# Kernel optimization log

Hardware: AMD Instinct MI355X
Metric: run time of the kernel (lower is better)

Reference implementation:

```python
import jax, jax.numpy as jnp
import numpy as np

N = 8192
X_DIM = 256
Y_DIM = 256


def setup_inputs() -> dict:
    key = jax.random.key(0)
    kx, ky, kw = jax.random.split(key, 3)
    x_samples = jax.random.normal(kx, (N, X_DIM), dtype=jnp.float32)
    y_samples = jax.random.normal(ky, (N, Y_DIM), dtype=jnp.float32)
    # kaiming-uniform-ish init for the bilinear weight [x_dim, y_dim]
    bound = float(np.sqrt(6.0 / X_DIM))
    w = jax.random.uniform(kw, (X_DIM, Y_DIM), dtype=jnp.float32,
                           minval=-bound, maxval=bound)
    return {"x_samples": x_samples, "y_samples": y_samples, "w": w}


def reference(x_samples, y_samples, w):
    # Pairwise bilinear scores S[i, b] = x[i] @ W @ y[b]
    # (equivalent to the original's tiled einsum, without O(N^2*dim) tiles)
    n = y_samples.shape[0]
    xw = x_samples @ w                      # [N, y_dim]
    S = xw @ y_samples.T                    # [N, N], S[i, b]
    # T0[i] = S[i, i]; T1.logsumexp(dim=1)[b] = logsumexp_i S[i, b]
    t0_mean = jnp.mean(jnp.diagonal(S))
    lse_mean = jnp.mean(jax.nn.logsumexp(S, axis=0))
    lower_bound = t0_mean - (lse_mean - jnp.log(jnp.float32(n)))
    return lower_bound
```

## Files before the change

### kernel.cpp

```cpp
#include <hip/hip_runtime.h>

typedef __attribute__((ext_vector_type(8))) short bf16x8;
typedef __attribute__((ext_vector_type(4))) float f32x4;
typedef __attribute__((ext_vector_type(8))) int   i32x8;
typedef __attribute__((ext_vector_type(4))) int   i32x4;

union OpU { i32x8 v; i32x4 h[2]; };

__device__ __forceinline__ unsigned short f2bf(float f) {
    unsigned int u = __float_as_uint(f);
    u += 0x7fffu + ((u >> 16) & 1u);
    return (unsigned short)(u >> 16);
}

__global__ void cast_wy_kernel(const float* __restrict__ y, const float* __restrict__ w,
                               unsigned char* __restrict__ YQ, unsigned short* __restrict__ WT,
                               float* __restrict__ scal)
{
    int idx = blockIdx.x * 256 + threadIdx.x;
    const float4 yv = ((const float4*)y)[idx];
    int pk = __builtin_amdgcn_cvt_pk_fp8_f32(yv.x, yv.y, 0, 0);
    pk     = __builtin_amdgcn_cvt_pk_fp8_f32(yv.z, yv.w, pk, 1);
    ((int*)YQ)[idx] = pk;
    if (idx < 16384) {
        const float4 wv = ((const float4*)w)[idx];
        int k = idx >> 6;
        int n0 = (idx & 63) * 4;
        WT[(size_t)(n0 + 0) * 256 + k] = f2bf(wv.x);
        WT[(size_t)(n0 + 1) * 256 + k] = f2bf(wv.y);
        WT[(size_t)(n0 + 2) * 256 + k] = f2bf(wv.z);
        WT[(size_t)(n0 + 3) * 256 + k] = f2bf(wv.w);
    }
    if (idx == 0) {
        scal[0] = 0.f; scal[1] = 0.f;
        ((unsigned int*)scal)[2] = 0u;
    }
}

__global__ __launch_bounds__(256, 4)
void gemm0_kernel(const float* __restrict__ X, const unsigned short* __restrict__ WT,
                  unsigned char* __restrict__ XWQ)
{
    __shared__ __align__(16) unsigned short As[64 * 64];
    __shared__ __align__(16) unsigned short Bs[64 * 64];

    const int tid  = threadIdx.x;
    const int lane = tid & 63;
    const int w    = tid >> 6;
    const int wm   = w >> 1, wn = w & 1;
    const int frow = lane & 15, quad = lane >> 4;
    const int rowBase = blockIdx.y * 64;
    const int colBase = blockIdx.x * 64;

    int aOff[2][2], bOff[2][2];
#pragma unroll
    for (int mi = 0; mi < 2; ++mi)
#pragma unroll
        for (int kk = 0; kk < 2; ++kk) {
            int ka = kk * 4 + quad;
            int ra = wm * 32 + mi * 16 + frow;
            aOff[mi][kk] = ra * 64 + ((ka ^ (ra & 7)) << 3);
            int rb = wn * 32 + mi * 16 + frow;
            bOff[mi][kk] = rb * 64 + ((ka ^ (rb & 7)) << 3);
        }

    f32x4 acc[2][2];
#pragma unroll
    for (int i = 0; i < 2; ++i)
#pragma unroll
        for (int j = 0; j < 2; ++j)
            acc[i][j] = f32x4{0.f, 0.f, 0.f, 0.f};

#pragma unroll
    for (int kt = 0; kt < 4; ++kt) {
        const int k0 = kt * 64;
#pragma unroll
        for (int it = 0; it < 2; ++it) {
            int p  = it * 256 + tid;
            int r  = p >> 3;
            int s  = p & 7;
            int kc = s ^ (r & 7);
            const unsigned short* gb = WT + (size_t)(colBase + r) * 256 + k0 + (kc << 3);
            __builtin_amdgcn_global_load_lds(
                (const __attribute__((address_space(1))) void*)gb,
                (__attribute__((address_space(3))) void*)&Bs[p << 3], 16, 0, 0);
        }
#pragma unroll
        for (int it = 0; it < 4; ++it) {
            int fidx = it * 256 + tid;
            int r  = fidx >> 4;
            int c4 = fidx & 15;
            float4 v = *(const float4*)&X[(size_t)(rowBase + r) * 256 + k0 + c4 * 4];
            ushort4 u;
            u.x = f2bf(v.x); u.y = f2bf(v.y); u.z = f2bf(v.z); u.w = f2bf(v.w);
            int slot = (c4 >> 1) ^ (r & 7);
            *(ushort4*)&As[r * 64 + (slot << 3) + (c4 & 1) * 4] = u;
        }
        __syncthreads();
#pragma unroll
        for (int kk = 0; kk < 2; ++kk) {
            bf16x8 a[2], b[2];
#pragma unroll
            for (int mi = 0; mi < 2; ++mi) a[mi] = *(const bf16x8*)&As[aOff[mi][kk]];
#pragma unroll
            for (int ni = 0; ni < 2; ++ni) b[ni] = *(const bf16x8*)&Bs[bOff[ni][kk]];
#pragma unroll
            for (int mi = 0; mi < 2; ++mi)
#pragma unroll
                for (int ni = 0; ni < 2; ++ni)
                    acc[mi][ni] = __builtin_amdgcn_mfma_f32_16x16x32_bf16(
                        a[mi], b[ni], acc[mi][ni], 0, 0, 0);
        }
        __syncthreads();
    }

#pragma unroll
    for (int mi = 0; mi < 2; ++mi)
#pragma unroll
        for (int ni = 0; ni < 2; ++ni)
#pragma unroll
            for (int r2 = 0; r2 < 4; ++r2) {
                int row = rowBase + wm * 32 + mi * 16 + quad * 4 + r2;
                int col = colBase + wn * 32 + ni * 16 + frow;
                float v = acc[mi][ni][r2];
                int q = __builtin_amdgcn_cvt_pk_fp8_f32(v, v, 0, 0);
                XWQ[(size_t)row * 256 + col] = (unsigned char)(q & 0xff);
            }
}

__global__ __launch_bounds__(256, 3)
void gemm1_kernel(const unsigned char* __restrict__ A,
                  const unsigned char* __restrict__ B,
                  float* __restrict__ P, float* __restrict__ scal)
{
    __shared__ __align__(16) unsigned char As[128 * 128];
    __shared__ __align__(16) unsigned char Bs[128 * 128];
    __shared__ float lsebuf[256];

    const int tid  = threadIdx.x;
    const int lane = tid & 63;
    const int w    = tid >> 6;
    const int wm   = w >> 1, wn = w & 1;
    const int frow = lane & 15, quad = lane >> 4;
    const int rowBase = blockIdx.y * 128;
    const int colBase = blockIdx.x * 128;

    f32x4 acc[4][4];
#pragma unroll
    for (int i = 0; i < 4; ++i)
#pragma unroll
        for (int j = 0; j < 4; ++j)
            acc[i][j] = f32x4{0.f, 0.f, 0.f, 0.f};

#pragma unroll
    for (int kt = 0; kt < 2; ++kt) {
        const int k0 = kt * 128;
#pragma unroll
        for (int it = 0; it < 4; ++it) {
            int p  = it * 256 + tid;
            int r  = p >> 3;
            int s  = p & 7;
            int kc = s ^ (r & 7);
            const unsigned char* ga = A + (size_t)(rowBase + r) * 256 + k0 + (kc << 4);
            const unsigned char* gb = B + (size_t)(colBase + r) * 256 + k0 + (kc << 4);
            __builtin_amdgcn_global_load_lds(
                (const __attribute__((address_space(1))) void*)ga,
                (__attribute__((address_space(3))) void*)&As[p << 4], 16, 0, 0);
            __builtin_amdgcn_global_load_lds(
                (const __attribute__((address_space(1))) void*)gb,
                (__attribute__((address_space(3))) void*)&Bs[p << 4], 16, 0, 0);
        }
        __syncthreads();

        const int c0 = quad * 2;
        i32x8 a[4], b[4];
#pragma unroll
        for (int mi = 0; mi < 4; ++mi) {
            int ra = wm * 64 + mi * 16 + frow;
            OpU u;
            u.h[0] = *(const i32x4*)&As[ra * 128 + ((c0 ^ (ra & 7)) << 4)];
            u.h[1] = *(const i32x4*)&As[ra * 128 + (((c0 + 1) ^ (ra & 7)) << 4)];
            a[mi] = u.v;
        }
#pragma unroll
        for (int ni = 0; ni < 4; ++ni) {
            int rb = wn * 64 + ni * 16 + frow;
            OpU u;
            u.h[0] = *(const i32x4*)&Bs[rb * 128 + ((c0 ^ (rb & 7)) << 4)];
            u.h[1] = *(const i32x4*)&Bs[rb * 128 + (((c0 + 1) ^ (rb & 7)) << 4)];
            b[ni] = u.v;
        }
#pragma unroll
        for (int mi = 0; mi < 4; ++mi)
#pragma unroll
            for (int ni = 0; ni < 4; ++ni)
                acc[mi][ni] = __builtin_amdgcn_mfma_scale_f32_16x16x128_f8f6f4(
                    a[mi], b[ni], acc[mi][ni],
                    0, 0,
                    0, 0x7f7f7f7f,
                    0, 0x7f7f7f7f);
        __syncthreads();
    }

#pragma unroll
    for (int ni = 0; ni < 4; ++ni) {
        float m = -1e30f;
#pragma unroll
        for (int mi = 0; mi < 4; ++mi)
#pragma unroll
            for (int r2 = 0; r2 < 4; ++r2) m = fmaxf(m, acc[mi][ni][r2]);
        m = fmaxf(m, __shfl_xor(m, 16));
        m = fmaxf(m, __shfl_xor(m, 32));
        float ssum = 0.f;
#pragma unroll
        for (int mi = 0; mi < 4; ++mi)
#pragma unroll
            for (int r2 = 0; r2 < 4; ++r2) ssum += __expf(acc[mi][ni][r2] - m);
        ssum += __shfl_xor(ssum, 16);
        ssum += __shfl_xor(ssum, 32);
        if (quad == 0)
            lsebuf[wm * 128 + wn * 64 + ni * 16 + frow] = m + __logf(ssum);
    }
    if (blockIdx.x == blockIdx.y && wm == wn) {
        float v = 0.f;
#pragma unroll
        for (int mi = 0; mi < 4; ++mi)
#pragma unroll
            for (int r2 = 0; r2 < 4; ++r2)
                if (quad * 4 + r2 == frow) v += acc[mi][mi][r2];
#pragma unroll
        for (int o = 1; o < 64; o <<= 1) v += __shfl_xor(v, o);
        if (lane == 0) atomicAdd(&scal[0], v);
    }
    __syncthreads();
    if (tid < 128) {
        float a = lsebuf[tid], b = lsebuf[128 + tid];
        float mm = fmaxf(a, b);
        P[(size_t)blockIdx.y * 8192 + colBase + tid]
            = mm + __logf(__expf(a - mm) + __expf(b - mm));
    }
}

__global__ void combine_kernel(const float* __restrict__ P, float* __restrict__ scal,
                               float* __restrict__ out)
{
    __shared__ float red[256];
    const int tid = threadIdx.x;
    const int col = blockIdx.x * 256 + tid;
    float m = -1e30f, s = 0.f;
#pragma unroll 8
    for (int j = 0; j < 64; ++j) {
        float v = P[(size_t)j * 8192 + col];
        float nm = fmaxf(m, v);
        s = s * __expf(m - nm) + __expf(v - nm);
        m = nm;
    }
    red[tid] = m + logf(s);
    __syncthreads();
#pragma unroll
    for (int o = 128; o > 0; o >>= 1) {
        if (tid < o) red[tid] += red[tid + o];
        __syncthreads();
    }
    if (tid == 0) {
        atomicAdd(&scal[1], red[0]);
        __threadfence();
        unsigned int old = __hip_atomic_fetch_add((unsigned int*)&scal[2], 1u,
                                                  __ATOMIC_ACQ_REL, __HIP_MEMORY_SCOPE_AGENT);
        if (old == 31u) {
            float t0 = __hip_atomic_load(&scal[0], __ATOMIC_RELAXED, __HIP_MEMORY_SCOPE_AGENT);
            float ls = __hip_atomic_load(&scal[1], __ATOMIC_RELAXED, __HIP_MEMORY_SCOPE_AGENT);
            const float invN = 1.f / 8192.f;
            out[0] = t0 * invN - (ls * invN - logf(8192.f));
        }
    }
}

extern "C" void kernel_launch(void* const* d_in, const int* in_sizes, int n_in,
                              void* d_out, int out_size, void* d_ws, size_t ws_size,
                              hipStream_t stream)
{
    const float* x = (const float*)d_in[0];
    const float* y = (const float*)d_in[1];
    const float* w = (const float*)d_in[2];
    float* out = (float*)d_out;

    char* ws = (char*)d_ws;
    unsigned char*  YQ  = (unsigned char*)(ws);
    unsigned char*  XWQ = (unsigned char*)(ws + 0x200000);
    unsigned short* WT  = (unsigned short*)(ws + 0x400000);
    float*          P   = (float*)        (ws + 0x420000);
    float*          scal= (float*)        (ws + 0x620000);

    cast_wy_kernel<<<2048, 256, 0, stream>>>(y, w, YQ, WT, scal);
    gemm0_kernel<<<dim3(4, 128), 256, 0, stream>>>(x, WT, XWQ);
    gemm1_kernel<<<dim3(64, 64), 256, 0, stream>>>(XWQ, YQ, P, scal);
    combine_kernel<<<32, 256, 0, stream>>>(P, scal, out);
}
```

Before: 111.7 us.

## Fuse cast and combine kernels into the two GEMM kernels

```diff
diff --git a/kernel.cpp b/kernel.cpp
--- a/kernel.cpp
+++ b/kernel.cpp
@@ -13,33 +13,11 @@
     return (unsigned short)(u >> 16);
 }
 
-__global__ void cast_wy_kernel(const float* __restrict__ y, const float* __restrict__ w,
-                               unsigned char* __restrict__ YQ, unsigned short* __restrict__ WT,
-                               float* __restrict__ scal)
-{
-    int idx = blockIdx.x * 256 + threadIdx.x;
-    const float4 yv = ((const float4*)y)[idx];
-    int pk = __builtin_amdgcn_cvt_pk_fp8_f32(yv.x, yv.y, 0, 0);
-    pk     = __builtin_amdgcn_cvt_pk_fp8_f32(yv.z, yv.w, pk, 1);
-    ((int*)YQ)[idx] = pk;
-    if (idx < 16384) {
-        const float4 wv = ((const float4*)w)[idx];
-        int k = idx >> 6;
-        int n0 = (idx & 63) * 4;
-        WT[(size_t)(n0 + 0) * 256 + k] = f2bf(wv.x);
-        WT[(size_t)(n0 + 1) * 256 + k] = f2bf(wv.y);
-        WT[(size_t)(n0 + 2) * 256 + k] = f2bf(wv.z);
-        WT[(size_t)(n0 + 3) * 256 + k] = f2bf(wv.w);
-    }
-    if (idx == 0) {
-        scal[0] = 0.f; scal[1] = 0.f;
-        ((unsigned int*)scal)[2] = 0u;
-    }
-}
-
 __global__ __launch_bounds__(256, 4)
-void gemm0_kernel(const float* __restrict__ X, const unsigned short* __restrict__ WT,
-                  unsigned char* __restrict__ XWQ)
+void gemm0_kernel(const float* __restrict__ X, const float* __restrict__ W,
+                  const float* __restrict__ Y,
+                  unsigned char* __restrict__ XWQ, unsigned char* __restrict__ YQ,
+                  float* __restrict__ scal, unsigned int* __restrict__ tick)
 {
     __shared__ __align__(16) unsigned short As[64 * 64];
     __shared__ __align__(16) unsigned short Bs[64 * 64];
@@ -51,6 +29,21 @@
     const int frow = lane & 15, quad = lane >> 4;
     const int rowBase = blockIdx.y * 64;
     const int colBase = blockIdx.x * 64;
+    const int lb = blockIdx.y * 4 + blockIdx.x;
+
+    if (lb == 0 && tid == 0) {
+        scal[0] = 0.f; scal[1] = 0.f;
+        tick[0] = 0u;  tick[1] = 0u;
+    }
+
+#pragma unroll
+    for (int it = 0; it < 4; ++it) {
+        int idx = lb * 1024 + it * 256 + tid;
+        const float4 yv = ((const float4*)Y)[idx];
+        int pk = __builtin_amdgcn_cvt_pk_fp8_f32(yv.x, yv.y, 0, 0);
+        pk     = __builtin_amdgcn_cvt_pk_fp8_f32(yv.z, yv.w, pk, 1);
+        ((int*)YQ)[idx] = pk;
+    }
 
     int aOff[2][2], bOff[2][2];
 #pragma unroll
@@ -74,17 +67,6 @@
 #pragma unroll
     for (int kt = 0; kt < 4; ++kt) {
         const int k0 = kt * 64;
-#pragma unroll
-        for (int it = 0; it < 2; ++it) {
-            int p  = it * 256 + tid;
-            int r  = p >> 3;
-            int s  = p & 7;
-            int kc = s ^ (r & 7);
-            const unsigned short* gb = WT + (size_t)(colBase + r) * 256 + k0 + (kc << 3);
-            __builtin_amdgcn_global_load_lds(
-                (const __attribute__((address_space(1))) void*)gb,
-                (__attribute__((address_space(3))) void*)&Bs[p << 3], 16, 0, 0);
-        }
 #pragma unroll
         for (int it = 0; it < 4; ++it) {
             int fidx = it * 256 + tid;
@@ -96,6 +78,21 @@
             int slot = (c4 >> 1) ^ (r & 7);
             *(ushort4*)&As[r * 64 + (slot << 3) + (c4 & 1) * 4] = u;
         }
+#pragma unroll
+        for (int it = 0; it < 4; ++it) {
+            int fidx = it * 256 + tid;
+            int k  = fidx >> 4;
+            int c4 = fidx & 15;
+            float4 v = *(const float4*)&W[(size_t)(k0 + k) * 256 + colBase + c4 * 4];
+            int c = k >> 3;
+            int kl = k & 7;
+#pragma unroll
+            for (int j = 0; j < 4; ++j) {
+                int n = c4 * 4 + j;
+                float vj = (j == 0) ? v.x : (j == 1) ? v.y : (j == 2) ? v.z : v.w;
+                Bs[n * 64 + ((c ^ (n & 7)) << 3) + kl] = f2bf(vj);
+            }
+        }
         __syncthreads();
 #pragma unroll
         for (int kk = 0; kk < 2; ++kk) {
@@ -131,11 +128,13 @@
 __global__ __launch_bounds__(256, 3)
 void gemm1_kernel(const unsigned char* __restrict__ A,
                   const unsigned char* __restrict__ B,
-                  float* __restrict__ P, float* __restrict__ scal)
+                  float* __restrict__ P, float* __restrict__ scal,
+                  unsigned int* __restrict__ tick, float* __restrict__ out)
 {
     __shared__ __align__(16) unsigned char As[128 * 128];
     __shared__ __align__(16) unsigned char Bs[128 * 128];
     __shared__ float lsebuf[256];
+    __shared__ unsigned int tkS;
 
     const int tid  = threadIdx.x;
     const int lane = tid & 63;
@@ -239,39 +238,51 @@
         P[(size_t)blockIdx.y * 8192 + colBase + tid]
             = mm + __logf(__expf(a - mm) + __expf(b - mm));
     }
-}
-
-__global__ void combine_kernel(const float* __restrict__ P, float* __restrict__ scal,
-                               float* __restrict__ out)
-{
-    __shared__ float red[256];
-    const int tid = threadIdx.x;
-    const int col = blockIdx.x * 256 + tid;
-    float m = -1e30f, s = 0.f;
+    __syncthreads();
+
+    if (tid == 0) {
+        __threadfence();
+        tkS = __hip_atomic_fetch_add(&tick[0], 1u, __ATOMIC_ACQ_REL,
+                                     __HIP_MEMORY_SCOPE_AGENT);
+    }
+    __syncthreads();
+    unsigned int t = tkS;
+    if (t >= 4064u) {
+        if (tid == 0) {
+            while (__hip_atomic_load(&tick[0], __ATOMIC_ACQUIRE,
+                                     __HIP_MEMORY_SCOPE_AGENT) < 4096u)
+                __builtin_amdgcn_s_sleep(8);
+        }
+        __syncthreads();
+        const int col = (int)(t - 4064u) * 256 + tid;
+        float m = -1e30f, s = 0.f;
 #pragma unroll 8
-    for (int j = 0; j < 64; ++j) {
-        float v = P[(size_t)j * 8192 + col];
-        float nm = fmaxf(m, v);
-        s = s * __expf(m - nm) + __expf(v - nm);
-        m = nm;
-    }
-    red[tid] = m + logf(s);
-    __syncthreads();
-#pragma unroll
-    for (int o = 128; o > 0; o >>= 1) {
-        if (tid < o) red[tid] += red[tid + o];
-        __syncthreads();
-    }
-    if (tid == 0) {
-        atomicAdd(&scal[1], red[0]);
-        __threadfence();
-        unsigned int old = __hip_atomic_fetch_add((unsigned int*)&scal[2], 1u,
-                                                  __ATOMIC_ACQ_REL, __HIP_MEMORY_SCOPE_AGENT);
-        if (old == 31u) {
-            float t0 = __hip_atomic_load(&scal[0], __ATOMIC_RELAXED, __HIP_MEMORY_SCOPE_AGENT);
-            float ls = __hip_atomic_load(&scal[1], __ATOMIC_RELAXED, __HIP_MEMORY_SCOPE_AGENT);
-            const float invN = 1.f / 8192.f;
-            out[0] = t0 * invN - (ls * invN - logf(8192.f));
+        for (int j = 0; j < 64; ++j) {
+            float v = P[(size_t)j * 8192 + col];
+            float nm = fmaxf(m, v);
+            s = s * __expf(m - nm) + __expf(v - nm);
+            m = nm;
+        }
+        lsebuf[tid] = m + logf(s);
+        __syncthreads();
+#pragma unroll
+        for (int o = 128; o > 0; o >>= 1) {
+            if (tid < o) lsebuf[tid] += lsebuf[tid + o];
+            __syncthreads();
+        }
+        if (tid == 0) {
+            atomicAdd(&scal[1], lsebuf[0]);
+            __threadfence();
+            unsigned int t2 = __hip_atomic_fetch_add(&tick[1], 1u, __ATOMIC_ACQ_REL,
+                                                     __HIP_MEMORY_SCOPE_AGENT);
+            if (t2 == 31u) {
+                float t0 = __hip_atomic_load(&scal[0], __ATOMIC_ACQUIRE,
+                                             __HIP_MEMORY_SCOPE_AGENT);
+                float ls = __hip_atomic_load(&scal[1], __ATOMIC_ACQUIRE,
+                                             __HIP_MEMORY_SCOPE_AGENT);
+                const float invN = 1.f / 8192.f;
+                out[0] = t0 * invN - (ls * invN - logf(8192.f));
+            }
         }
     }
 }
@@ -286,14 +297,12 @@
     float* out = (float*)d_out;
 
     char* ws = (char*)d_ws;
-    unsigned char*  YQ  = (unsigned char*)(ws);
-    unsigned char*  XWQ = (unsigned char*)(ws + 0x200000);
-    unsigned short* WT  = (unsigned short*)(ws + 0x400000);
-    float*          P   = (float*)        (ws + 0x420000);
-    float*          scal= (float*)        (ws + 0x620000);
-
-    cast_wy_kernel<<<2048, 256, 0, stream>>>(y, w, YQ, WT, scal);
-    gemm0_kernel<<<dim3(4, 128), 256, 0, stream>>>(x, WT, XWQ);
-    gemm1_kernel<<<dim3(64, 64), 256, 0, stream>>>(XWQ, YQ, P, scal);
-    combine_kernel<<<32, 256, 0, stream>>>(P, scal, out);
+    unsigned char* XWQ = (unsigned char*)(ws);
+    unsigned char* YQ  = (unsigned char*)(ws + 0x200000);
+    float*         P   = (float*)        (ws + 0x400000);
+    float*         scal= (float*)        (ws + 0x600000);
+    unsigned int*  tick= (unsigned int*) (ws + 0x600010);
+
+    gemm0_kernel<<<dim3(4, 128), 256, 0, stream>>>(x, w, y, XWQ, YQ, scal, tick);
+    gemm1_kernel<<<dim3(64, 64), 256, 0, stream>>>(XWQ, YQ, P, scal, tick, out);
 }
```

New measurement: 242.7 us. 2.17x slower.
